# Performance work log

Measured on AMD Instinct MI355X. Metric: run time of the kernel, lower is better.

Reference implementation:

```python
import jax, jax.numpy as jnp
import numpy as np

B, D = 4096, 128
LU, LI = 10, 20
NU, NI = 100000, 100000
NFU, NFI = 2000, 5000
MARGIN = 1.0


def setup_inputs() -> dict:
    key = jax.random.key(0)
    ks = jax.random.split(key, 32)
    s = 0.05
    n = lambda i, shape: (jax.random.normal(ks[i], shape, dtype=jnp.float32) * s)
    inp = {
        'user_indices': jax.random.randint(ks[0], (B,), 0, NU),
        'user_feat': jax.random.randint(ks[1], (B, LU), 0, NFU),
        'pos_item_indices': jax.random.randint(ks[2], (B,), 0, NI),
        'pos_item_feat': jax.random.randint(ks[3], (B, LI), 0, NFI),
        'neg_item_indices': jax.random.randint(ks[4], (B, 1), 0, NI),
        'neg_item_feat': jax.random.randint(ks[5], (B, 1, LI), 0, NFI),
        'comp_neg_indices': jax.random.randint(ks[6], (B,), 0, NI),
        'eps': jax.random.normal(ks[7], (B, D), dtype=jnp.float32),
        # learned parameters
        'emb_user': n(8, (NU, D)),
        'emb_item': n(9, (NI, D)),
        'emb_feat_user': n(10, (NFU, D)).at[0].set(0.0),  # row 0 is padding
        'emb_feat_item': n(11, (NFI, D)).at[0].set(0.0),
        'pop_emb_user': n(12, (D,)),
        'int_emb_user': n(13, (D,)),
        'pop_emb_item': n(14, (D,)),
        'int_emb_item': n(15, (D,)),
        'W_pop': n(16, (D, D)), 'b_pop': jnp.zeros((D,), jnp.float32),
        'W_int': n(17, (D, D)), 'b_int': jnp.zeros((D,), jnp.float32),
        'enc_W': n(18, (LI * D, D)), 'enc_b': jnp.zeros((D,), jnp.float32),
        'dec_W': n(19, (D, LI * D)), 'dec_b': jnp.zeros((LI * D,), jnp.float32),
        'fc11_W': n(20, (D, D)), 'fc11_b': jnp.zeros((D,), jnp.float32),
        'fc12_W': n(21, (D, D)), 'fc12_b': jnp.zeros((D,), jnp.float32),
    }
    return inp


def _attend_pool(fuse, feat_mask, vec, W, b):
    # fuse: [B, L+1, D], feat_mask: [B, L+1] (int, 0 = padded)
    scores = jnp.einsum('bld,d->bl', fuse, vec)
    scores = jnp.where(feat_mask == 0, -jnp.inf, scores)
    w = jax.nn.softmax(scores, axis=1)
    pooled = jnp.einsum('bld,bl->bd', fuse, w)
    return pooled @ W + b


def _branch(idx, feat, emb_table, feat_table, pop_vec, int_vec, W_pop, b_pop, W_int, b_int):
    e = emb_table[idx]                       # [B, D]
    fe = feat_table[feat]                    # [B, L, D]
    fuse = jnp.concatenate([e[:, None, :], fe], axis=1)           # [B, L+1, D]
    ones = jnp.ones((idx.shape[0], 1), dtype=feat.dtype)
    mask = jnp.concatenate([ones, feat], axis=1)                  # [B, L+1]
    hot = _attend_pool(fuse, mask, pop_vec, W_pop, b_pop)
    cold = _attend_pool(fuse, mask, int_vec, W_int, b_int)
    return hot, cold, e, fe


def reference(user_indices, user_feat, pos_item_indices, pos_item_feat,
              neg_item_indices, neg_item_feat, comp_neg_indices, eps,
              emb_user, emb_item, emb_feat_user, emb_feat_item,
              pop_emb_user, int_emb_user, pop_emb_item, int_emb_item,
              W_pop, b_pop, W_int, b_int,
              enc_W, enc_b, dec_W, dec_b, fc11_W, fc11_b, fc12_W, fc12_b):
    neg_item_indices = neg_item_indices.squeeze(1)
    neg_item_feat = neg_item_feat.squeeze(1)

    u_hot, u_cold, _, _ = _branch(user_indices, user_feat, emb_user, emb_feat_user,
                                  pop_emb_user, int_emb_user, W_pop, b_pop, W_int, b_int)
    p_hot, p_cold, pos_e, pos_fe = _branch(pos_item_indices, pos_item_feat, emb_item, emb_feat_item,
                                           pop_emb_item, int_emb_item, W_pop, b_pop, W_int, b_int)
    n_hot, n_cold, _, _ = _branch(neg_item_indices, neg_item_feat, emb_item, emb_feat_item,
                                  pop_emb_item, int_emb_item, W_pop, b_pop, W_int, b_int)

    loss_hot = jax.nn.relu(jnp.sum((u_hot - p_hot) ** 2, -1)
                           - jnp.sum((u_hot - n_hot) ** 2, -1) + MARGIN)
    loss_cold = jax.nn.relu(jnp.sum((u_cold - p_cold) ** 2, -1)
                            - jnp.sum((u_cold - n_cold) ** 2, -1) + MARGIN)

    # VAE over positive item feature embeddings
    x = pos_fe.reshape(pos_fe.shape[0], LI * D)
    h1 = jax.nn.relu(x @ enc_W + enc_b)
    mu = h1 @ fc11_W + fc11_b
    logvar = h1 @ fc12_W + fc12_b
    z = eps * jnp.exp(0.5 * logvar) + mu
    recon = z @ dec_W + dec_b                                    # [B, LI*D]
    mse = jnp.sum((recon - x) ** 2)
    kld = -0.5 * jnp.sum(1.0 + logvar - mu ** 2 - jnp.exp(logvar))
    vae_l = mse / LI + kld

    comp_e = emb_item[comp_neg_indices]
    mmi = -jnp.sum(jax.nn.log_sigmoid(jnp.sum(z * pos_e, 1) - jnp.sum(z * comp_e, 1)))
    item_vae_loss = mmi + vae_l + jnp.sum((z - pos_e) ** 2)

    return loss_hot, loss_cold, item_vae_loss
```

## Files before the change

kernel.cpp:

```cpp
#include <hip/hip_runtime.h>
#include <math.h>

#define BATCH 4096
#define DIM 128
#define LU 10
#define LI 20

typedef float  f32x4  __attribute__((ext_vector_type(4)));
typedef short  s16x8  __attribute__((ext_vector_type(8)));

__device__ __forceinline__ short f2bf(float x) {
    unsigned u = __float_as_uint(x);
    u += 0x7FFFu + ((u >> 16) & 1u);
    return (short)(u >> 16);
}

__global__ __launch_bounds__(256) void k_prep(
    const float* __restrict__ enc_W, const float* __restrict__ dec_W,
    const float* __restrict__ fc11_W, const float* __restrict__ fc12_W,
    const float* __restrict__ W_pop, const float* __restrict__ W_int,
    const float* __restrict__ ef_item,
    short* __restrict__ encWT, short* __restrict__ decWT,
    short* __restrict__ fc11WT, short* __restrict__ fc12WT,
    short* __restrict__ wpopT, short* __restrict__ wintT,
    short* __restrict__ ef16)
{
    __shared__ float tile[32][33];
    const int b = blockIdx.x;
    const int t = threadIdx.x;

    if (b < 704) {
        const float* src; short* dst; int r0, c0, src_ld, dst_ld;
        if (b < 320) {
            int tk = b % 80, tj = b / 80;
            src = enc_W; dst = encWT; r0 = tk * 32; c0 = tj * 32; src_ld = 128; dst_ld = 2560;
        } else if (b < 640) {
            int tb = b - 320; int tc = tb % 80, td = tb / 80;
            src = dec_W; dst = decWT; r0 = td * 32; c0 = tc * 32; src_ld = 2560; dst_ld = 128;
        } else if (b < 656) {
            int tb = b - 640; int tk = tb % 4, tj = tb / 4;
            src = fc11_W; dst = fc11WT; r0 = tk * 32; c0 = tj * 32; src_ld = 128; dst_ld = 128;
        } else if (b < 672) {
            int tb = b - 656; int tk = tb % 4, tj = tb / 4;
            src = fc12_W; dst = fc12WT; r0 = tk * 32; c0 = tj * 32; src_ld = 128; dst_ld = 128;
        } else if (b < 688) {
            int tb = b - 672; int tk = tb % 4, tj = tb / 4;
            src = W_pop; dst = wpopT; r0 = tk * 32; c0 = tj * 32; src_ld = 128; dst_ld = 128;
        } else {
            int tb = b - 688; int tk = tb % 4, tj = tb / 4;
            src = W_int; dst = wintT; r0 = tk * 32; c0 = tj * 32; src_ld = 128; dst_ld = 128;
        }
        for (int q = 0; q < 4; ++q) {
            int e = t + q * 256;
            int r = e >> 5, c = e & 31;
            tile[r][c] = src[(size_t)(r0 + r) * src_ld + (c0 + c)];
        }
        __syncthreads();
        for (int q = 0; q < 4; ++q) {
            int e = t + q * 256;
            int r = e >> 5, c = e & 31;
            dst[(size_t)(c0 + r) * dst_ld + (r0 + c)] = f2bf(tile[c][r]);
        }
    } else {
        int base = (b - 704) * 1024 + t * 4;
        float4 v = *(const float4*)(ef_item + base);
        short4 o;
        o.x = f2bf(v.x); o.y = f2bf(v.y); o.z = f2bf(v.z); o.w = f2bf(v.w);
        *(short4*)(ef16 + base) = o;
    }
}

template<int L>
__device__ __forceinline__ void pool_reg(
    const int* __restrict__ idxp, const int* __restrict__ featp,
    const float* __restrict__ etab, const float* __restrict__ ftab,
    const float* __restrict__ vpop, const float* __restrict__ vint,
    float* __restrict__ poolH, float* __restrict__ poolC,
    int i, int j32)
{
    const int d = j32 * 4;
    const float4 vp = *(const float4*)(vpop + d);
    const float4 vi = *(const float4*)(vint + d);

    float4 r[L + 1];
    const int idx = idxp[i];
    r[0] = *(const float4*)(etab + (size_t)idx * DIM + d);
    unsigned mbits = 1u;
#pragma unroll
    for (int l = 0; l < L; ++l) {
        int f = featp[(size_t)i * L + l];
        mbits |= (f != 0 ? 2u : 0u) << l;
        r[l + 1] = *(const float4*)(ftab + (size_t)f * DIM + d);
    }

    float sp[L + 1], si[L + 1];
#pragma unroll
    for (int l = 0; l <= L; ++l) {
        sp[l] = r[l].x * vp.x + r[l].y * vp.y + r[l].z * vp.z + r[l].w * vp.w;
        si[l] = r[l].x * vi.x + r[l].y * vi.y + r[l].z * vi.z + r[l].w * vi.w;
    }

#pragma unroll
    for (int l = 0; l <= L; ++l) {
        float a = sp[l], b = si[l];
        a += __shfl_xor(a, 1, 64);  b += __shfl_xor(b, 1, 64);
        a += __shfl_xor(a, 2, 64);  b += __shfl_xor(b, 2, 64);
        a += __shfl_xor(a, 4, 64);  b += __shfl_xor(b, 4, 64);
        a += __shfl_xor(a, 8, 64);  b += __shfl_xor(b, 8, 64);
        a += __shfl_xor(a, 16, 64); b += __shfl_xor(b, 16, 64);
        sp[l] = a; si[l] = b;
    }

    float mh = sp[0], mc = si[0];
#pragma unroll
    for (int l = 1; l <= L; ++l) {
        bool v = (mbits >> l) & 1u;
        mh = v ? fmaxf(mh, sp[l]) : mh;
        mc = v ? fmaxf(mc, si[l]) : mc;
    }
    float sh = 0.f, sc = 0.f;
#pragma unroll
    for (int l = 0; l <= L; ++l) {
        bool v = (mbits >> l) & 1u;
        float eh = v ? __expf(sp[l] - mh) : 0.f;
        float ec = v ? __expf(si[l] - mc) : 0.f;
        sp[l] = eh; si[l] = ec;
        sh += eh; sc += ec;
    }
    const float rh = 1.f / sh, rc = 1.f / sc;

    float hx = sp[0] * r[0].x, hy = sp[0] * r[0].y, hz = sp[0] * r[0].z, hw = sp[0] * r[0].w;
    float cx = si[0] * r[0].x, cy = si[0] * r[0].y, cz = si[0] * r[0].z, cw = si[0] * r[0].w;
#pragma unroll
    for (int l = 1; l <= L; ++l) {
        float wh = sp[l], wc = si[l];
        hx += wh * r[l].x; hy += wh * r[l].y; hz += wh * r[l].z; hw += wh * r[l].w;
        cx += wc * r[l].x; cy += wc * r[l].y; cz += wc * r[l].z; cw += wc * r[l].w;
    }
    float4 oH; oH.x = hx * rh; oH.y = hy * rh; oH.z = hz * rh; oH.w = hw * rh;
    float4 oC; oC.x = cx * rc; oC.y = cy * rc; oC.z = cz * rc; oC.w = cw * rc;
    *(float4*)(poolH + (size_t)i * DIM + d) = oH;
    *(float4*)(poolC + (size_t)i * DIM + d) = oC;
}

__global__ __launch_bounds__(512) void k_main(
    const int* __restrict__ user_idx, const int* __restrict__ user_feat,
    const int* __restrict__ pos_idx,  const int* __restrict__ pos_feat,
    const int* __restrict__ neg_idx,  const int* __restrict__ neg_feat,
    const int* __restrict__ comp_idx,
    const float* __restrict__ emb_user, const float* __restrict__ emb_item,
    const float* __restrict__ ef_user,  const float* __restrict__ ef_item,
    const float* __restrict__ pop_u, const float* __restrict__ int_u,
    const float* __restrict__ pop_i, const float* __restrict__ int_i,
    const float* __restrict__ eps,
    const float* __restrict__ enc_b, const float* __restrict__ dec_b,
    const float* __restrict__ fc11_b, const float* __restrict__ fc12_b,
    const short* __restrict__ encWT, const short* __restrict__ decWT,
    const short* __restrict__ fc11WT, const short* __restrict__ fc12WT,
    const short* __restrict__ ef16,
    float* __restrict__ pooled, float* __restrict__ vae_part)
{
    __shared__ int   featsL[320];
    __shared__ int   spi[16], sci[16];
    __shared__ __align__(16) short hlds[2048];
    __shared__ float xbuf[16][128];
    __shared__ float sdots[4][16][3];
    __shared__ float red[512];

    const int t    = threadIdx.x;
    const int w    = t >> 6;
    const int lane = t & 63;
    const int g    = lane >> 4;
    const int q    = lane & 15;
    const size_t SEC = (size_t)BATCH * DIM;

    if (blockIdx.x >= 256) {
        const int pb  = blockIdx.x - 256;
        const int br  = pb >> 8;
        const int i   = (pb & 255) * 16 + (t >> 5);
        const int j32 = t & 31;
        if (br == 0) {
            pool_reg<LU>(user_idx, user_feat, emb_user, ef_user, pop_u, int_u,
                         pooled + 0 * SEC, pooled + 1 * SEC, i, j32);
        } else if (br == 1) {
            pool_reg<LI>(pos_idx, pos_feat, emb_item, ef_item, pop_i, int_i,
                         pooled + 2 * SEC, pooled + 3 * SEC, i, j32);
        } else {
            pool_reg<LI>(neg_idx, neg_feat, emb_item, ef_item, pop_i, int_i,
                         pooled + 4 * SEC, pooled + 5 * SEC, i, j32);
        }
        return;
    }

    const int i0   = blockIdx.x * 16;
    const int wcol = w & 3;
    const int wpar = w >> 2;

    if (t < 16)      spi[t] = pos_idx[i0 + t];
    else if (t < 32) sci[t - 16] = comp_idx[i0 + t - 16];
    if (t < 320) featsL[t] = pos_feat[i0 * LI + t];
    __syncthreads();

    const int j0 = wcol * 32 + q;
    const int j1 = j0 + 16;
    const short* bbase0 = encWT + (size_t)j0 * 2560 + g * 8;
    const short* bbase1 = encWT + (size_t)j1 * 2560 + g * 8;

    f32x4 acc0 = {0.f, 0.f, 0.f, 0.f};
    f32x4 acc1 = {0.f, 0.f, 0.f, 0.f};
    for (int l = wpar; l < LI; l += 2) {
        const int f = featsL[q * LI + l];
        const short* arow = ef16 + (size_t)f * DIM + g * 8;
#pragma unroll
        for (int dt = 0; dt < 4; ++dt) {
            const int koff = l * 128 + dt * 32;
            s16x8 a  = *(const s16x8*)(arow + dt * 32);
            s16x8 b0 = *(const s16x8*)(bbase0 + koff);
            s16x8 b1 = *(const s16x8*)(bbase1 + koff);
            acc0 = __builtin_amdgcn_mfma_f32_16x16x32_bf16(a, b0, acc0, 0, 0, 0);
            acc1 = __builtin_amdgcn_mfma_f32_16x16x32_bf16(a, b1, acc1, 0, 0, 0);
        }
    }

    if (wpar == 1) {
#pragma unroll
        for (int r = 0; r < 4; ++r) {
            int s = g * 4 + r;
            xbuf[s][j0] = acc0[r];
            xbuf[s][j1] = acc1[r];
        }
    }
    __syncthreads();
    if (wpar == 0) {
        float eb0 = enc_b[j0], eb1 = enc_b[j1];
#pragma unroll
        for (int r = 0; r < 4; ++r) {
            int s = g * 4 + r;
            float h0 = acc0[r] + xbuf[s][j0] + eb0; h0 = h0 > 0.f ? h0 : 0.f;
            float h1 = acc1[r] + xbuf[s][j1] + eb1; h1 = h1 > 0.f ? h1 : 0.f;
            int swz = (s & 7) << 3;
            hlds[(s * 128 + j0) ^ swz] = f2bf(h0);
            hlds[(s * 128 + j1) ^ swz] = f2bf(h1);
        }
    }
    __syncthreads();

    const short* WT  = (wpar == 0) ? fc11WT : fc12WT;
    const short* fb0 = WT + (size_t)j0 * DIM + g * 8;
    const short* fb1 = WT + (size_t)j1 * DIM + g * 8;
    f32x4 r0v = {0.f,0.f,0.f,0.f}, r1v = {0.f,0.f,0.f,0.f};
#pragma unroll
    for (int kt = 0; kt < 4; ++kt) {
        int sidx = (q * 128 + kt * 32 + g * 8) ^ ((q & 7) << 3);
        s16x8 a  = *(const s16x8*)&hlds[sidx];
        s16x8 w0 = *(const s16x8*)(fb0 + kt * 32);
        s16x8 w1 = *(const s16x8*)(fb1 + kt * 32);
        r0v = __builtin_amdgcn_mfma_f32_16x16x32_bf16(a, w0, r0v, 0, 0, 0);
        r1v = __builtin_amdgcn_mfma_f32_16x16x32_bf16(a, w1, r1v, 0, 0, 0);
    }
    if (wpar == 1) {
        float b12_0 = fc12_b[j0], b12_1 = fc12_b[j1];
#pragma unroll
        for (int r = 0; r < 4; ++r) {
            int s = g * 4 + r;
            xbuf[s][j0] = r0v[r] + b12_0;
            xbuf[s][j1] = r1v[r] + b12_1;
        }
    }
    __syncthreads();

    float kacc = 0.f;
    if (wpar == 0) {
        float b11_0 = fc11_b[j0], b11_1 = fc11_b[j1];
#pragma unroll
        for (int r = 0; r < 4; ++r) {
            const int s = g * 4 + r;
            const int i = i0 + s;
            float m0 = r0v[r] + b11_0, m1 = r1v[r] + b11_1;
            float v0 = xbuf[s][j0],    v1 = xbuf[s][j1];
            float e0 = eps[(size_t)i * DIM + j0];
            float e1 = eps[(size_t)i * DIM + j1];
            float z0 = e0 * expf(0.5f * v0) + m0;
            float z1 = e1 * expf(0.5f * v1) + m1;
            int swz = (s & 7) << 3;
            hlds[(s * 128 + j0) ^ swz] = f2bf(z0);
            hlds[(s * 128 + j1) ^ swz] = f2bf(z1);
            kacc += (1.f + v0 - m0 * m0 - expf(v0)) + (1.f + v1 - m1 * m1 - expf(v1));

            const size_t pb2 = (size_t)spi[s] * DIM;
            const size_t cb2 = (size_t)sci[s] * DIM;
            float pe0 = emb_item[pb2 + j0], pe1 = emb_item[pb2 + j1];
            float ce0 = emb_item[cb2 + j0], ce1 = emb_item[cb2 + j1];
            float zp = z0 * pe0 + z1 * pe1;
            float zc = z0 * ce0 + z1 * ce1;
            float d0 = z0 - pe0, d1 = z1 - pe1;
            float zq = d0 * d0 + d1 * d1;
            for (int mm = 8; mm >= 1; mm >>= 1) {
                zp += __shfl_xor(zp, mm, 64);
                zc += __shfl_xor(zc, mm, 64);
                zq += __shfl_xor(zq, mm, 64);
            }
            if (q == 0) {
                sdots[w][s][0] = zp;
                sdots[w][s][1] = zc;
                sdots[w][s][2] = zq;
            }
        }
    }
    __syncthreads();

    s16x8 za[4];
#pragma unroll
    for (int kt = 0; kt < 4; ++kt)
        za[kt] = *(const s16x8*)&hlds[(q * 128 + kt * 32 + g * 8) ^ ((q & 7) << 3)];

    const int cw = w * 320;
    float macc = 0.f;
    for (int fp = 0; fp < 10; ++fp) {
        const int c0 = cw + fp * 32 + q;
        const int c1 = c0 + 16;
        const short* bp0 = decWT + (size_t)c0 * DIM + g * 8;
        const short* bp1 = decWT + (size_t)c1 * DIM + g * 8;
        s16x8 b0[4], b1[4];
#pragma unroll
        for (int kt = 0; kt < 4; ++kt) {
            b0[kt] = *(const s16x8*)(bp0 + kt * 32);
            b1[kt] = *(const s16x8*)(bp1 + kt * 32);
        }
        const int l0 = c0 >> 7, d0 = c0 & 127;
        const int l1 = c1 >> 7, d1 = c1 & 127;
        float x0[4], x1[4];
#pragma unroll
        for (int r = 0; r < 4; ++r) {
            x0[r] = ef_item[(size_t)featsL[(g * 4 + r) * LI + l0] * DIM + d0];
            x1[r] = ef_item[(size_t)featsL[(g * 4 + r) * LI + l1] * DIM + d1];
        }
        const float bias0 = dec_b[c0], bias1 = dec_b[c1];
        f32x4 a0 = {0.f,0.f,0.f,0.f}, a1 = {0.f,0.f,0.f,0.f};
#pragma unroll
        for (int kt = 0; kt < 4; ++kt) {
            a0 = __builtin_amdgcn_mfma_f32_16x16x32_bf16(za[kt], b0[kt], a0, 0, 0, 0);
            a1 = __builtin_amdgcn_mfma_f32_16x16x32_bf16(za[kt], b1[kt], a1, 0, 0, 0);
        }
#pragma unroll
        for (int r = 0; r < 4; ++r) {
            float dd0 = a0[r] + bias0 - x0[r];
            float dd1 = a1[r] + bias1 - x1[r];
            macc += dd0 * dd0 + dd1 * dd1;
        }
    }

    red[t] = 0.05f * macc + ((wpar == 0) ? -0.5f * kacc : 0.f);
    __syncthreads();
    if (t < 16) {
        float zp = 0.f, zc = 0.f, zq = 0.f;
        for (int ww = 0; ww < 4; ++ww) {
            zp += sdots[ww][t][0];
            zc += sdots[ww][t][1];
            zq += sdots[ww][t][2];
        }
        float x = zp - zc;
        float ls = (x >= 0.f) ? -log1pf(expf(-x)) : (x - log1pf(expf(x)));
        red[t] += -ls + zq;
    }
    __syncthreads();
    for (int off = 256; off > 0; off >>= 1) {
        if (t < off) red[t] += red[t + off];
        __syncthreads();
    }
    if (t == 0) vae_part[blockIdx.x] = red[0];
}

__global__ __launch_bounds__(256) void k_loss(
    const float* __restrict__ pooled,
    const short* __restrict__ wpopT, const short* __restrict__ wintT,
    const float* __restrict__ vae_part,
    float* __restrict__ out_hot, float* __restrict__ out_cold,
    float* __restrict__ out_scalar)
{
    __shared__ float sArr[4][16];
    __shared__ float red[256];

    const int t    = threadIdx.x;
    const int w    = t >> 6;
    const int lane = t & 63;
    const int g    = lane >> 4;
    const int q    = lane & 15;
    const int i0   = blockIdx.x * 16;

    const int h     = w >> 1;
    const int other = (w & 1) + 1;
    const float* pu = pooled + (size_t)(0 * 2 + h) * BATCH * DIM;
    const float* po = pooled + (size_t)(other * 2 + h) * BATCH * DIM;
    const short* wT = h ? wintT : wpopT;

    s16x8 afr[4];
#pragma unroll
    for (int kt = 0; kt < 4; ++kt) {
        const size_t off = (size_t)(i0 + q) * DIM + kt * 32 + g * 8;
        f32x4 ua = *(const f32x4*)(pu + off);
        f32x4 ub = *(const f32x4*)(pu + off + 4);
        f32x4 oa = *(const f32x4*)(po + off);
        f32x4 ob = *(const f32x4*)(po + off + 4);
        s16x8 v;
        v[0] = f2bf(ua[0] - oa[0]); v[1] = f2bf(ua[1] - oa[1]);
        v[2] = f2bf(ua[2] - oa[2]); v[3] = f2bf(ua[3] - oa[3]);
        v[4] = f2bf(ub[0] - ob[0]); v[5] = f2bf(ub[1] - ob[1]);
        v[6] = f2bf(ub[2] - ob[2]); v[7] = f2bf(ub[3] - ob[3]);
        afr[kt] = v;
    }

    float sq0 = 0.f, sq1 = 0.f, sq2 = 0.f, sq3 = 0.f;
    for (int fr = 0; fr < 8; ++fr) {
        const short* bb = wT + (size_t)(fr * 16 + q) * DIM + g * 8;
        f32x4 acc = {0.f, 0.f, 0.f, 0.f};
#pragma unroll
        for (int kt = 0; kt < 4; ++kt) {
            s16x8 bfr = *(const s16x8*)(bb + kt * 32);
            acc = __builtin_amdgcn_mfma_f32_16x16x32_bf16(afr[kt], bfr, acc, 0, 0, 0);
        }
        sq0 += acc[0] * acc[0]; sq1 += acc[1] * acc[1];
        sq2 += acc[2] * acc[2]; sq3 += acc[3] * acc[3];
    }
    for (int m = 8; m >= 1; m >>= 1) {
        sq0 += __shfl_xor(sq0, m, 64);
        sq1 += __shfl_xor(sq1, m, 64);
        sq2 += __shfl_xor(sq2, m, 64);
        sq3 += __shfl_xor(sq3, m, 64);
    }
    if (q == 0) {
        sArr[w][g * 4 + 0] = sq0;
        sArr[w][g * 4 + 1] = sq1;
        sArr[w][g * 4 + 2] = sq2;
        sArr[w][g * 4 + 3] = sq3;
    }
    __syncthreads();
    if (t < 16) {
        float v = sArr[0][t] - sArr[1][t] + 1.0f;
        out_hot[i0 + t] = v > 0.f ? v : 0.f;
    } else if (t < 32) {
        int s = t - 16;
        float v = sArr[2][s] - sArr[3][s] + 1.0f;
        out_cold[i0 + s] = v > 0.f ? v : 0.f;
    }

    if (blockIdx.x == 0) {
        red[t] = vae_part[t];
        __syncthreads();
        for (int off = 128; off > 0; off >>= 1) {
            if (t < off) red[t] += red[t + off];
            __syncthreads();
        }
        if (t == 0) out_scalar[0] = red[0];
    }
}

extern "C" void kernel_launch(void* const* d_in, const int* in_sizes, int n_in,
                              void* d_out, int out_size, void* d_ws, size_t ws_size,
                              hipStream_t stream) {
    const int*   user_idx  = (const int*)d_in[0];
    const int*   user_feat = (const int*)d_in[1];
    const int*   pos_idx   = (const int*)d_in[2];
    const int*   pos_feat  = (const int*)d_in[3];
    const int*   neg_idx   = (const int*)d_in[4];
    const int*   neg_feat  = (const int*)d_in[5];
    const int*   comp_idx  = (const int*)d_in[6];
    const float* eps       = (const float*)d_in[7];
    const float* emb_user  = (const float*)d_in[8];
    const float* emb_item  = (const float*)d_in[9];
    const float* ef_user   = (const float*)d_in[10];
    const float* ef_item   = (const float*)d_in[11];
    const float* pop_u     = (const float*)d_in[12];
    const float* int_u     = (const float*)d_in[13];
    const float* pop_i     = (const float*)d_in[14];
    const float* int_i     = (const float*)d_in[15];
    const float* W_pop     = (const float*)d_in[16];
    const float* W_int     = (const float*)d_in[18];
    const float* enc_W     = (const float*)d_in[20];
    const float* enc_b     = (const float*)d_in[21];
    const float* dec_W     = (const float*)d_in[22];
    const float* dec_b     = (const float*)d_in[23];
    const float* fc11_W    = (const float*)d_in[24];
    const float* fc11_b    = (const float*)d_in[25];
    const float* fc12_W    = (const float*)d_in[26];
    const float* fc12_b    = (const float*)d_in[27];

    float* out = (float*)d_out;
    char*  ws  = (char*)d_ws;

    short* encWT    = (short*)(ws);
    short* decWT    = (short*)(ws + 655360);
    short* fc11WT   = (short*)(ws + 1310720);
    short* fc12WT   = (short*)(ws + 1343488);
    short* wpopT    = (short*)(ws + 1376256);
    short* wintT    = (short*)(ws + 1409024);
    short* ef16     = (short*)(ws + 1441792);
    float* pooled   = (float*)(ws + 2721792);
    float* vae_part = (float*)(ws + 15304704);

    k_prep<<<dim3(1329), dim3(256), 0, stream>>>(
        enc_W, dec_W, fc11_W, fc12_W, W_pop, W_int, ef_item,
        encWT, decWT, fc11WT, fc12WT, wpopT, wintT, ef16);

    k_main<<<dim3(1024), dim3(512), 0, stream>>>(
        user_idx, user_feat, pos_idx, pos_feat, neg_idx, neg_feat, comp_idx,
        emb_user, emb_item, ef_user, ef_item,
        pop_u, int_u, pop_i, int_i,
        eps, enc_b, dec_b, fc11_b, fc12_b,
        encWT, decWT, fc11WT, fc12WT, ef16,
        pooled, vae_part);

    k_loss<<<dim3(256), dim3(256), 0, stream>>>(
        pooled, wpopT, wintT, vae_part,
        out, out + BATCH, out + 2 * BATCH);
}
```

Measured before the change: 92.70 us.

## Precompute per-row feature attention scores and gather bf16 features in pooling

The prep kernel now converts the user feature table to bf16. It also computes, once per table row, the dot products of every feature-table row with the pop and int vectors. Pooling then looks these scores up instead of recomputing dot products per gathered feature, and accumulates from bf16 rows with one wave per sample. This cuts the gather bytes and the shuffle reductions in the memory-bound pooling path, at the cost of extra prep work over the whole tables and reduced precision in the pooled features.

```diff
diff --git a/kernel.cpp b/kernel.cpp
--- a/kernel.cpp
+++ b/kernel.cpp
@@ -19,11 +19,15 @@
     const float* __restrict__ enc_W, const float* __restrict__ dec_W,
     const float* __restrict__ fc11_W, const float* __restrict__ fc12_W,
     const float* __restrict__ W_pop, const float* __restrict__ W_int,
-    const float* __restrict__ ef_item,
+    const float* __restrict__ ef_item, const float* __restrict__ ef_user,
+    const float* __restrict__ pop_i, const float* __restrict__ int_i,
+    const float* __restrict__ pop_u, const float* __restrict__ int_u,
     short* __restrict__ encWT, short* __restrict__ decWT,
     short* __restrict__ fc11WT, short* __restrict__ fc12WT,
     short* __restrict__ wpopT, short* __restrict__ wintT,
-    short* __restrict__ ef16)
+    short* __restrict__ ef16, short* __restrict__ efU16,
+    float* __restrict__ projIP, float* __restrict__ projII,
+    float* __restrict__ projUP, float* __restrict__ projUI)
 {
     __shared__ float tile[32][33];
     const int b = blockIdx.x;
@@ -61,55 +65,91 @@
             int r = e >> 5, c = e & 31;
             dst[(size_t)(c0 + r) * dst_ld + (r0 + c)] = f2bf(tile[c][r]);
         }
-    } else {
+    } else if (b < 1329) {
         int base = (b - 704) * 1024 + t * 4;
         float4 v = *(const float4*)(ef_item + base);
         short4 o;
         o.x = f2bf(v.x); o.y = f2bf(v.y); o.z = f2bf(v.z); o.w = f2bf(v.w);
         *(short4*)(ef16 + base) = o;
+    } else if (b < 1579) {
+        int base = (b - 1329) * 1024 + t * 4;
+        float4 v = *(const float4*)(ef_user + base);
+        short4 o;
+        o.x = f2bf(v.x); o.y = f2bf(v.y); o.z = f2bf(v.z); o.w = f2bf(v.w);
+        *(short4*)(efU16 + base) = o;
+    } else {
+        const int pb = b - 1579;
+        const float* tab; const float* v0p; const float* v1p;
+        float* o0; float* o1; int row;
+        if (pb < 625) {
+            row = pb * 8 + (t >> 5);
+            tab = ef_item; v0p = pop_i; v1p = int_i; o0 = projIP; o1 = projII;
+        } else {
+            row = (pb - 625) * 8 + (t >> 5);
+            tab = ef_user; v0p = pop_u; v1p = int_u; o0 = projUP; o1 = projUI;
+        }
+        const int d = (t & 31) * 4;
+        float4 rv = *(const float4*)(tab + (size_t)row * DIM + d);
+        float4 a  = *(const float4*)(v0p + d);
+        float4 c  = *(const float4*)(v1p + d);
+        float s0 = rv.x * a.x + rv.y * a.y + rv.z * a.z + rv.w * a.w;
+        float s1 = rv.x * c.x + rv.y * c.y + rv.z * c.z + rv.w * c.w;
+        s0 += __shfl_xor(s0, 1, 64);  s1 += __shfl_xor(s1, 1, 64);
+        s0 += __shfl_xor(s0, 2, 64);  s1 += __shfl_xor(s1, 2, 64);
+        s0 += __shfl_xor(s0, 4, 64);  s1 += __shfl_xor(s1, 4, 64);
+        s0 += __shfl_xor(s0, 8, 64);  s1 += __shfl_xor(s1, 8, 64);
+        s0 += __shfl_xor(s0, 16, 64); s1 += __shfl_xor(s1, 16, 64);
+        if ((t & 31) == 0) { o0[row] = s0; o1[row] = s1; }
     }
 }
 
 template<int L>
-__device__ __forceinline__ void pool_reg(
+__device__ __forceinline__ void pool_sc(
     const int* __restrict__ idxp, const int* __restrict__ featp,
-    const float* __restrict__ etab, const float* __restrict__ ftab,
+    const float* __restrict__ etab, const unsigned short* __restrict__ ftab16,
+    const float* __restrict__ projP, const float* __restrict__ projI,
     const float* __restrict__ vpop, const float* __restrict__ vint,
     float* __restrict__ poolH, float* __restrict__ poolC,
-    int i, int j32)
+    int i_in, int lane)
 {
-    const int d = j32 * 4;
-    const float4 vp = *(const float4*)(vpop + d);
-    const float4 vi = *(const float4*)(vint + d);
-
-    float4 r[L + 1];
-    const int idx = idxp[i];
-    r[0] = *(const float4*)(etab + (size_t)idx * DIM + d);
+    const int i = __builtin_amdgcn_readfirstlane(i_in);
+    const int d = lane * 2;
+
+    int fidx[L];
+#pragma unroll
+    for (int l = 0; l < L; ++l) fidx[l] = featp[i * L + l];
+    const int idx0 = idxp[i];
+
+    const float2 e0 = *(const float2*)(etab + (size_t)idx0 * DIM + d);
+    unsigned rr[L];
+#pragma unroll
+    for (int l = 0; l < L; ++l)
+        rr[l] = *(const unsigned*)(ftab16 + (size_t)fidx[l] * DIM + d);
+
+    float sp[L + 1], si[L + 1];
+#pragma unroll
+    for (int l = 0; l < L; ++l) {
+        sp[l + 1] = projP[fidx[l]];
+        si[l + 1] = projI[fidx[l]];
+    }
+
+    {
+        const float2 vp = *(const float2*)(vpop + d);
+        const float2 vi = *(const float2*)(vint + d);
+        float aH = e0.x * vp.x + e0.y * vp.y;
+        float aC = e0.x * vi.x + e0.y * vi.y;
+        aH += __shfl_xor(aH, 1, 64);  aC += __shfl_xor(aC, 1, 64);
+        aH += __shfl_xor(aH, 2, 64);  aC += __shfl_xor(aC, 2, 64);
+        aH += __shfl_xor(aH, 4, 64);  aC += __shfl_xor(aC, 4, 64);
+        aH += __shfl_xor(aH, 8, 64);  aC += __shfl_xor(aC, 8, 64);
+        aH += __shfl_xor(aH, 16, 64); aC += __shfl_xor(aC, 16, 64);
+        aH += __shfl_xor(aH, 32, 64); aC += __shfl_xor(aC, 32, 64);
+        sp[0] = aH; si[0] = aC;
+    }
+
     unsigned mbits = 1u;
 #pragma unroll
-    for (int l = 0; l < L; ++l) {
-        int f = featp[(size_t)i * L + l];
-        mbits |= (f != 0 ? 2u : 0u) << l;
-        r[l + 1] = *(const float4*)(ftab + (size_t)f * DIM + d);
-    }
-
-    float sp[L + 1], si[L + 1];
-#pragma unroll
-    for (int l = 0; l <= L; ++l) {
-        sp[l] = r[l].x * vp.x + r[l].y * vp.y + r[l].z * vp.z + r[l].w * vp.w;
-        si[l] = r[l].x * vi.x + r[l].y * vi.y + r[l].z * vi.z + r[l].w * vi.w;
-    }
-
-#pragma unroll
-    for (int l = 0; l <= L; ++l) {
-        float a = sp[l], b = si[l];
-        a += __shfl_xor(a, 1, 64);  b += __shfl_xor(b, 1, 64);
-        a += __shfl_xor(a, 2, 64);  b += __shfl_xor(b, 2, 64);
-        a += __shfl_xor(a, 4, 64);  b += __shfl_xor(b, 4, 64);
-        a += __shfl_xor(a, 8, 64);  b += __shfl_xor(b, 8, 64);
-        a += __shfl_xor(a, 16, 64); b += __shfl_xor(b, 16, 64);
-        sp[l] = a; si[l] = b;
-    }
+    for (int l = 0; l < L; ++l) mbits |= (fidx[l] != 0 ? 2u : 0u) << l;
 
     float mh = sp[0], mc = si[0];
 #pragma unroll
@@ -121,7 +161,7 @@
     float sh = 0.f, sc = 0.f;
 #pragma unroll
     for (int l = 0; l <= L; ++l) {
-        bool v = (mbits >> l) & 1u;
+        bool v = (l == 0) | ((mbits >> l) & 1u);
         float eh = v ? __expf(sp[l] - mh) : 0.f;
         float ec = v ? __expf(si[l] - mc) : 0.f;
         sp[l] = eh; si[l] = ec;
@@ -129,27 +169,28 @@
     }
     const float rh = 1.f / sh, rc = 1.f / sc;
 
-    float hx = sp[0] * r[0].x, hy = sp[0] * r[0].y, hz = sp[0] * r[0].z, hw = sp[0] * r[0].w;
-    float cx = si[0] * r[0].x, cy = si[0] * r[0].y, cz = si[0] * r[0].z, cw = si[0] * r[0].w;
-#pragma unroll
-    for (int l = 1; l <= L; ++l) {
-        float wh = sp[l], wc = si[l];
-        hx += wh * r[l].x; hy += wh * r[l].y; hz += wh * r[l].z; hw += wh * r[l].w;
-        cx += wc * r[l].x; cy += wc * r[l].y; cz += wc * r[l].z; cw += wc * r[l].w;
-    }
-    float4 oH; oH.x = hx * rh; oH.y = hy * rh; oH.z = hz * rh; oH.w = hw * rh;
-    float4 oC; oC.x = cx * rc; oC.y = cy * rc; oC.z = cz * rc; oC.w = cw * rc;
-    *(float4*)(poolH + (size_t)i * DIM + d) = oH;
-    *(float4*)(poolC + (size_t)i * DIM + d) = oC;
+    float hx = sp[0] * e0.x, hy = sp[0] * e0.y;
+    float cx = si[0] * e0.x, cy = si[0] * e0.y;
+#pragma unroll
+    for (int l = 0; l < L; ++l) {
+        float x = __uint_as_float(rr[l] << 16);
+        float y = __uint_as_float(rr[l] & 0xFFFF0000u);
+        hx += sp[l + 1] * x; hy += sp[l + 1] * y;
+        cx += si[l + 1] * x; cy += si[l + 1] * y;
+    }
+    float2 oH; oH.x = hx * rh; oH.y = hy * rh;
+    float2 oC; oC.x = cx * rc; oC.y = cy * rc;
+    *(float2*)(poolH + (size_t)i * DIM + d) = oH;
+    *(float2*)(poolC + (size_t)i * DIM + d) = oC;
 }
 
-__global__ __launch_bounds__(512) void k_main(
+__global__ __launch_bounds__(512) void k_AB(
     const int* __restrict__ user_idx, const int* __restrict__ user_feat,
     const int* __restrict__ pos_idx,  const int* __restrict__ pos_feat,
     const int* __restrict__ neg_idx,  const int* __restrict__ neg_feat,
     const int* __restrict__ comp_idx,
     const float* __restrict__ emb_user, const float* __restrict__ emb_item,
-    const float* __restrict__ ef_user,  const float* __restrict__ ef_item,
+    const float* __restrict__ ef_item,
     const float* __restrict__ pop_u, const float* __restrict__ int_u,
     const float* __restrict__ pop_i, const float* __restrict__ int_i,
     const float* __restrict__ eps,
@@ -157,7 +198,9 @@
     const float* __restrict__ fc11_b, const float* __restrict__ fc12_b,
     const short* __restrict__ encWT, const short* __restrict__ decWT,
     const short* __restrict__ fc11WT, const short* __restrict__ fc12WT,
-    const short* __restrict__ ef16,
+    const short* __restrict__ ef16, const short* __restrict__ efU16,
+    const float* __restrict__ projIP, const float* __restrict__ projII,
+    const float* __restrict__ projUP, const float* __restrict__ projUI,
     float* __restrict__ pooled, float* __restrict__ vae_part)
 {
     __shared__ int   featsL[320];
@@ -175,19 +218,24 @@
     const size_t SEC = (size_t)BATCH * DIM;
 
     if (blockIdx.x >= 256) {
-        const int pb  = blockIdx.x - 256;
-        const int br  = pb >> 8;
-        const int i   = (pb & 255) * 16 + (t >> 5);
-        const int j32 = t & 31;
+        const int pb = blockIdx.x - 256;
+        const int br = pb % 3;
+        const int i  = (pb / 3) * 8 + w;
         if (br == 0) {
-            pool_reg<LU>(user_idx, user_feat, emb_user, ef_user, pop_u, int_u,
-                         pooled + 0 * SEC, pooled + 1 * SEC, i, j32);
+            pool_sc<LU>(user_idx, user_feat, emb_user,
+                        (const unsigned short*)efU16, projUP, projUI,
+                        pop_u, int_u,
+                        pooled + 0 * SEC, pooled + 1 * SEC, i, lane);
         } else if (br == 1) {
-            pool_reg<LI>(pos_idx, pos_feat, emb_item, ef_item, pop_i, int_i,
-                         pooled + 2 * SEC, pooled + 3 * SEC, i, j32);
+            pool_sc<LI>(pos_idx, pos_feat, emb_item,
+                        (const unsigned short*)ef16, projIP, projII,
+                        pop_i, int_i,
+                        pooled + 2 * SEC, pooled + 3 * SEC, i, lane);
         } else {
-            pool_reg<LI>(neg_idx, neg_feat, emb_item, ef_item, pop_i, int_i,
-                         pooled + 4 * SEC, pooled + 5 * SEC, i, j32);
+            pool_sc<LI>(neg_idx, neg_feat, emb_item,
+                        (const unsigned short*)ef16, projIP, projII,
+                        pop_i, int_i,
+                        pooled + 4 * SEC, pooled + 5 * SEC, i, lane);
         }
         return;
     }
@@ -277,7 +325,7 @@
             const int s = g * 4 + r;
             const int i = i0 + s;
             float m0 = r0v[r] + b11_0, m1 = r1v[r] + b11_1;
-            float v0 = xbuf[s][j0],    v1 = xbuf[s][j1];
+            float v0 = xbuf[s][j0],  v1 = xbuf[s][j1];
             float e0 = eps[(size_t)i * DIM + j0];
             float e1 = eps[(size_t)i * DIM + j1];
             float z0 = e0 * expf(0.5f * v0) + m0;
@@ -495,19 +543,27 @@
     short* wpopT    = (short*)(ws + 1376256);
     short* wintT    = (short*)(ws + 1409024);
     short* ef16     = (short*)(ws + 1441792);
-    float* pooled   = (float*)(ws + 2721792);
-    float* vae_part = (float*)(ws + 15304704);
-
-    k_prep<<<dim3(1329), dim3(256), 0, stream>>>(
-        enc_W, dec_W, fc11_W, fc12_W, W_pop, W_int, ef_item,
-        encWT, decWT, fc11WT, fc12WT, wpopT, wintT, ef16);
-
-    k_main<<<dim3(1024), dim3(512), 0, stream>>>(
+    short* efU16    = (short*)(ws + 2721792);
+    float* pooled   = (float*)(ws + 4282368);
+    float* vae_part = (float*)(ws + 16865280);
+    float* projIP   = (float*)(ws + 16874496);
+    float* projII   = (float*)(ws + 16894496);
+    float* projUP   = (float*)(ws + 16914496);
+    float* projUI   = (float*)(ws + 16922496);
+
+    k_prep<<<dim3(2454), dim3(256), 0, stream>>>(
+        enc_W, dec_W, fc11_W, fc12_W, W_pop, W_int, ef_item, ef_user,
+        pop_i, int_i, pop_u, int_u,
+        encWT, decWT, fc11WT, fc12WT, wpopT, wintT, ef16, efU16,
+        projIP, projII, projUP, projUI);
+
+    k_AB<<<dim3(1792), dim3(512), 0, stream>>>(
         user_idx, user_feat, pos_idx, pos_feat, neg_idx, neg_feat, comp_idx,
-        emb_user, emb_item, ef_user, ef_item,
+        emb_user, emb_item, ef_item,
         pop_u, int_u, pop_i, int_i,
         eps, enc_b, dec_b, fc11_b, fc12_b,
-        encWT, decWT, fc11WT, fc12WT, ef16,
+        encWT, decWT, fc11WT, fc12WT, ef16, efU16,
+        projIP, projII, projUP, projUI,
         pooled, vae_part);
 
     k_loss<<<dim3(256), dim3(256), 0, stream>>>(
```

After: 76.18 us. -17.8%, faster.
